# Kernel optimization log

Measured on AMD Instinct MI355X. Metric: run time of the kernel, lower is better.

The kernel has to match this reference:

```python
import jax, jax.numpy as jnp
import numpy as np

IN_DIM = 512
HID = IN_DIM // 2
N_SCENES = 64
SEG_LEN = 4096
N = N_SCENES * SEG_LEN
EPS = 1e-5


def setup_inputs() -> dict:
    key = jax.random.key(0)
    ks = jax.random.split(key, 6)
    feats = jax.random.normal(ks[0], (N, IN_DIM), dtype=jnp.float32)
    offsets = (jnp.arange(N_SCENES + 1, dtype=jnp.int32) * SEG_LEN)
    ln_g = jnp.ones((IN_DIM,), jnp.float32) + 0.02 * jax.random.normal(ks[1], (IN_DIM,), jnp.float32)
    ln_b = 0.02 * jax.random.normal(ks[2], (IN_DIM,), jnp.float32)
    w1 = jax.random.normal(ks[3], (HID, IN_DIM), jnp.float32) / np.sqrt(IN_DIM)
    b1 = jnp.zeros((HID,), jnp.float32)
    w2 = jax.random.normal(ks[4], (1, HID), jnp.float32) / np.sqrt(HID)
    b2 = jnp.zeros((1,), jnp.float32)
    return {"feats": feats, "ln_g": ln_g, "ln_b": ln_b, "w1": w1, "b1": b1, "w2": w2, "b2": b2, "offsets": offsets}


def reference(feats, ln_g, ln_b, w1, b1, w2, b2, offsets):
    n = feats.shape[0]
    # segment id per point from prefix-sum offsets
    seg = jnp.searchsorted(offsets, jnp.arange(n, dtype=offsets.dtype), side="right") - 1
    # score MLP: LayerNorm -> Linear -> GELU(exact) -> Linear -> scalar
    mu = jnp.mean(feats, axis=-1, keepdims=True)
    var = jnp.mean(jnp.square(feats - mu), axis=-1, keepdims=True)
    x = (feats - mu) * jax.lax.rsqrt(var + EPS) * ln_g + ln_b
    h = jax.nn.gelu(x @ w1.T + b1, approximate=False)  # [N, HID]
    s = (h @ w2.T + b2)[:, 0]  # [N]
    # segment softmax (stable)
    smax = jax.ops.segment_max(s, seg, num_segments=N_SCENES)
    e = jnp.exp(s - smax[seg])
    denom = jax.ops.segment_sum(e, seg, num_segments=N_SCENES)
    w = e / denom[seg]
    # weighted sum per segment -> [N_SCENES, IN_DIM]
    pooled = jax.ops.segment_sum(feats * w[:, None], seg, num_segments=N_SCENES)
    return pooled
```

## Files before the change

kernel.cpp:

```cpp
#include <hip/hip_runtime.h>

#define IN_DIM 512
#define HID_DIM 256

typedef __bf16 bf16x8 __attribute__((ext_vector_type(8)));
typedef unsigned short ushort8 __attribute__((ext_vector_type(8)));
typedef float floatx4 __attribute__((ext_vector_type(4)));

__device__ __forceinline__ unsigned short f2bf(float x) {
    unsigned int u = __float_as_uint(x);
    u += 0x7FFFu + ((u >> 16) & 1u);
    return (unsigned short)(u >> 16);
}

__global__ void conv_w1_kernel(const float* __restrict__ w1,
                               unsigned short* __restrict__ w1bf, int n) {
    int i = blockIdx.x * blockDim.x + threadIdx.x;
    if (i < n) w1bf[i] = f2bf(w1[i]);
}

#define XS_STRIDE 520

__global__ __launch_bounds__(256, 2) void score_kernel(
    const float* __restrict__ feats, const float* __restrict__ ln_g,
    const float* __restrict__ ln_b, const unsigned short* __restrict__ w1bf,
    const float* __restrict__ b1, const float* __restrict__ w2,
    const float* __restrict__ b2, float* __restrict__ s_out, int N) {
    __shared__ unsigned short xs[64][XS_STRIDE];
    __shared__ float spart[4][64];

    const int tid = threadIdx.x;
    const int wid = tid >> 6;
    const int lane = tid & 63;
    const int quad = lane >> 4;
    const int l16 = lane & 15;
    const int row0 = blockIdx.x * 64;
    const int c8 = lane * 8;

    const float4 g0 = *(const float4*)(ln_g + c8);
    const float4 g1 = *(const float4*)(ln_g + c8 + 4);
    const float4 h0 = *(const float4*)(ln_b + c8);
    const float4 h1 = *(const float4*)(ln_b + c8 + 4);

    for (int i = 0; i < 16; i += 2) {
        const int ra = (wid << 4) + i;
        const int rb = ra + 1;
        size_t rowa = (size_t)(row0 + ra);
        size_t rowb = (size_t)(row0 + rb);
        if (rowa >= (size_t)N) rowa = (size_t)N - 1;
        if (rowb >= (size_t)N) rowb = (size_t)N - 1;
        const float4 a0 = *(const float4*)(feats + rowa * IN_DIM + c8);
        const float4 a1 = *(const float4*)(feats + rowa * IN_DIM + c8 + 4);
        const float4 d0 = *(const float4*)(feats + rowb * IN_DIM + c8);
        const float4 d1 = *(const float4*)(feats + rowb * IN_DIM + c8 + 4);

        float sa = a0.x + a0.y + a0.z + a0.w + a1.x + a1.y + a1.z + a1.w;
        float qa = a0.x * a0.x + a0.y * a0.y + a0.z * a0.z + a0.w * a0.w +
                   a1.x * a1.x + a1.y * a1.y + a1.z * a1.z + a1.w * a1.w;
        float sb = d0.x + d0.y + d0.z + d0.w + d1.x + d1.y + d1.z + d1.w;
        float qb = d0.x * d0.x + d0.y * d0.y + d0.z * d0.z + d0.w * d0.w +
                   d1.x * d1.x + d1.y * d1.y + d1.z * d1.z + d1.w * d1.w;
        for (int m = 32; m; m >>= 1) {
            sa += __shfl_xor(sa, m);
            qa += __shfl_xor(qa, m);
            sb += __shfl_xor(sb, m);
            qb += __shfl_xor(qb, m);
        }
        const float mua = sa * (1.0f / IN_DIM);
        const float rsa = rsqrtf(qa * (1.0f / IN_DIM) - mua * mua + 1e-5f);
        const float mub = sb * (1.0f / IN_DIM);
        const float rsb = rsqrtf(qb * (1.0f / IN_DIM) - mub * mub + 1e-5f);

        ushort8 va, vb;
        va[0] = f2bf((a0.x - mua) * rsa * g0.x + h0.x);
        va[1] = f2bf((a0.y - mua) * rsa * g0.y + h0.y);
        va[2] = f2bf((a0.z - mua) * rsa * g0.z + h0.z);
        va[3] = f2bf((a0.w - mua) * rsa * g0.w + h0.w);
        va[4] = f2bf((a1.x - mua) * rsa * g1.x + h1.x);
        va[5] = f2bf((a1.y - mua) * rsa * g1.y + h1.y);
        va[6] = f2bf((a1.z - mua) * rsa * g1.z + h1.z);
        va[7] = f2bf((a1.w - mua) * rsa * g1.w + h1.w);
        vb[0] = f2bf((d0.x - mub) * rsb * g0.x + h0.x);
        vb[1] = f2bf((d0.y - mub) * rsb * g0.y + h0.y);
        vb[2] = f2bf((d0.z - mub) * rsb * g0.z + h0.z);
        vb[3] = f2bf((d0.w - mub) * rsb * g0.w + h0.w);
        vb[4] = f2bf((d1.x - mub) * rsb * g1.x + h1.x);
        vb[5] = f2bf((d1.y - mub) * rsb * g1.y + h1.y);
        vb[6] = f2bf((d1.z - mub) * rsb * g1.z + h1.z);
        vb[7] = f2bf((d1.w - mub) * rsb * g1.w + h1.w);
        *(ushort8*)&xs[ra][c8] = va;
        *(ushort8*)&xs[rb][c8] = vb;
    }
    __syncthreads();

    floatx4 acc[4][4];
#pragma unroll
    for (int rt = 0; rt < 4; rt++)
#pragma unroll
        for (int ht = 0; ht < 4; ht++) acc[rt][ht] = (floatx4)(0.0f);

    const int hbase = wid * 64;
    for (int kk = 0; kk < IN_DIM; kk += 32) {
        const int kc = kk + quad * 8;
        bf16x8 af[4], bf[4];
#pragma unroll
        for (int rt = 0; rt < 4; rt++) {
            af[rt] = __builtin_bit_cast(bf16x8, *(const ushort8*)&xs[rt * 16 + l16][kc]);
        }
#pragma unroll
        for (int ht = 0; ht < 4; ht++) {
            const int hid = hbase + ht * 16 + l16;
            bf[ht] = __builtin_bit_cast(bf16x8, *(const ushort8*)(w1bf + hid * IN_DIM + kc));
        }
#pragma unroll
        for (int rt = 0; rt < 4; rt++)
#pragma unroll
            for (int ht = 0; ht < 4; ht++)
                acc[rt][ht] = __builtin_amdgcn_mfma_f32_16x16x32_bf16(af[rt], bf[ht], acc[rt][ht], 0, 0, 0);
    }
    __syncthreads();

    float w2v[4], b1v[4];
#pragma unroll
    for (int ht = 0; ht < 4; ht++) {
        const int hid = hbase + ht * 16 + l16;
        w2v[ht] = w2[hid];
        b1v[ht] = b1[hid];
    }
    float p[4][4];
#pragma unroll
    for (int rt = 0; rt < 4; rt++) {
#pragma unroll
        for (int reg = 0; reg < 4; reg++) {
            float t = 0.0f;
#pragma unroll
            for (int ht = 0; ht < 4; ht++) {
                const float hv = acc[rt][ht][reg] + b1v[ht];
                t += 0.5f * hv * (1.0f + erff(hv * 0.70710678118654752f)) * w2v[ht];
            }
            p[rt][reg] = t;
        }
    }
#pragma unroll
    for (int m = 1; m < 16; m <<= 1)
#pragma unroll
        for (int rt = 0; rt < 4; rt++)
#pragma unroll
            for (int reg = 0; reg < 4; reg++) p[rt][reg] += __shfl_xor(p[rt][reg], m);
    if (l16 == 0) {
#pragma unroll
        for (int rt = 0; rt < 4; rt++)
#pragma unroll
            for (int reg = 0; reg < 4; reg++)
                spart[wid][rt * 16 + quad * 4 + reg] = p[rt][reg];
    }
    __syncthreads();
    if (tid < 64) {
        const int row = row0 + tid;
        if (row < N) {
            s_out[row] = spart[0][tid] + spart[1][tid] + spart[2][tid] + spart[3][tid] + b2[0];
        }
    }
}

__global__ void segstat_kernel(const float* __restrict__ s, const int* __restrict__ offsets,
                               float* __restrict__ smax, float* __restrict__ denom, int nseg) {
    const int seg = blockIdx.x;
    const int st = offsets[seg];
    const int en = offsets[seg + 1];
    const int tid = threadIdx.x;
    __shared__ float red[8];
    float m = -3.4e38f;
    for (int i = st + tid; i < en; i += 256) m = fmaxf(m, s[i]);
    for (int mm = 32; mm; mm >>= 1) m = fmaxf(m, __shfl_xor(m, mm));
    if ((tid & 63) == 0) red[tid >> 6] = m;
    __syncthreads();
    const float M = fmaxf(fmaxf(red[0], red[1]), fmaxf(red[2], red[3]));
    float sum = 0.0f;
    for (int i = st + tid; i < en; i += 256) sum += expf(s[i] - M);
    for (int mm = 32; mm; mm >>= 1) sum += __shfl_xor(sum, mm);
    if ((tid & 63) == 0) red[4 + (tid >> 6)] = sum;
    __syncthreads();
    if (tid == 0) {
        smax[seg] = M;
        denom[seg] = red[4] + red[5] + red[6] + red[7];
    }
}

#define CHUNK 512
__global__ __launch_bounds__(256) void pool_kernel(
    const float* __restrict__ feats, const float* __restrict__ s,
    const float* __restrict__ smax, const float* __restrict__ denom,
    const int* __restrict__ offsets, int nseg, float* __restrict__ out, int N) {
    __shared__ float wbuf[CHUNK];
    __shared__ int sbuf[CHUNK];
    const int tid = threadIdx.x;
    const int r0 = blockIdx.x * CHUNK;
    const int nrows = min(CHUNK, N - r0);

    for (int r = tid; r < CHUNK; r += 256) {
        const int row = r0 + r;
        float wv = 0.0f;
        int sg = 0;
        if (row < N) {
            int lo = 0, hi = nseg;
            while (hi - lo > 1) {
                const int mid = (lo + hi) >> 1;
                if (offsets[mid] <= row) lo = mid; else hi = mid;
            }
            sg = lo;
            wv = expf(s[row] - smax[sg]) / denom[sg];
        }
        wbuf[r] = wv;
        sbuf[r] = sg;
    }
    __syncthreads();

    const int seg0 = sbuf[0];
    const int segl = sbuf[nrows - 1];
    const int d = 2 * tid;
    if (seg0 == segl) {
        float ax = 0.0f, ay = 0.0f;
        const float* fp = feats + (size_t)r0 * IN_DIM + d;
#pragma unroll 8
        for (int r = 0; r < nrows; r++) {
            const float2 f = *(const float2*)(fp + (size_t)r * IN_DIM);
            const float wv = wbuf[r];
            ax += wv * f.x;
            ay += wv * f.y;
        }
        atomicAdd(&out[seg0 * IN_DIM + d], ax);
        atomicAdd(&out[seg0 * IN_DIM + d + 1], ay);
    } else {
        for (int r = 0; r < nrows; r++) {
            const float2 f = *(const float2*)(feats + (size_t)(r0 + r) * IN_DIM + d);
            const float wv = wbuf[r];
            const int sg = sbuf[r];
            if (wv != 0.0f) {
                atomicAdd(&out[sg * IN_DIM + d], wv * f.x);
                atomicAdd(&out[sg * IN_DIM + d + 1], wv * f.y);
            }
        }
    }
}

extern "C" void kernel_launch(void* const* d_in, const int* in_sizes, int n_in,
                              void* d_out, int out_size, void* d_ws, size_t ws_size,
                              hipStream_t stream) {
    const float* feats = (const float*)d_in[0];
    const float* ln_g = (const float*)d_in[1];
    const float* ln_b = (const float*)d_in[2];
    const float* w1 = (const float*)d_in[3];
    const float* b1 = (const float*)d_in[4];
    const float* w2 = (const float*)d_in[5];
    const float* b2 = (const float*)d_in[6];
    const int* offsets = (const int*)d_in[7];
    const int N = in_sizes[0] / IN_DIM;
    const int nseg = in_sizes[7] - 1;
    float* out = (float*)d_out;

    char* ws = (char*)d_ws;
    unsigned short* w1bf = (unsigned short*)ws;
    float* s_arr = (float*)(ws + (size_t)HID_DIM * IN_DIM * 2);
    float* smax = (float*)(ws + (size_t)HID_DIM * IN_DIM * 2 + (size_t)N * 4);
    float* denom = smax + nseg;

    hipMemsetAsync(d_out, 0, (size_t)out_size * sizeof(float), stream);
    conv_w1_kernel<<<(HID_DIM * IN_DIM + 255) / 256, 256, 0, stream>>>(w1, w1bf, HID_DIM * IN_DIM);
    score_kernel<<<(N + 63) / 64, 256, 0, stream>>>(feats, ln_g, ln_b, w1bf, b1, w2, b2, s_arr, N);
    segstat_kernel<<<nseg, 256, 0, stream>>>(s_arr, offsets, smax, denom, nseg);
    pool_kernel<<<(N + CHUNK - 1) / CHUNK, 256, 0, stream>>>(feats, s_arr, smax, denom, offsets, nseg, out, N);
}
```

Measured before the change: 943.3 us.

## Fold LayerNorm affine into W1 and apply normalization after the GEMM

Pre-multiplies W1 by the LayerNorm gain and precomputes per-hidden sums of the scaled weights and a combined bias that absorbs ln_b and b1. The score kernel now converts raw feats to bf16 without normalizing, and computes per-row mean and variance from the bf16 values read during the MFMA loop. It then applies mean subtraction and rsqrt scaling to the GEMM output in the epilogue, which removes the per-row shuffle reductions and per-element normalize math from the load phase. The trade is extra precision loss: bf16 rounding of un-normalized feats, statistics taken from bf16 values, and cancellation in acc minus mu times gw. The pool kernel chunk size is also halved to 256.

New measurement: 941.0 us. Within noise of the previous version (-0.2%).

```diff
diff --git a/kernel.cpp b/kernel.cpp
--- a/kernel.cpp
+++ b/kernel.cpp
@@ -2,32 +2,65 @@
 
 #define IN_DIM 512
 #define HID_DIM 256
+#define XS_STRIDE 520
 
 typedef __bf16 bf16x8 __attribute__((ext_vector_type(8)));
 typedef unsigned short ushort8 __attribute__((ext_vector_type(8)));
 typedef float floatx4 __attribute__((ext_vector_type(4)));
 
-__device__ __forceinline__ unsigned short f2bf(float x) {
+__device__ __forceinline__ unsigned short f2bf_rne(float x) {
     unsigned int u = __float_as_uint(x);
     u += 0x7FFFu + ((u >> 16) & 1u);
     return (unsigned short)(u >> 16);
 }
 
-__global__ void conv_w1_kernel(const float* __restrict__ w1,
-                               unsigned short* __restrict__ w1bf, int n) {
-    int i = blockIdx.x * blockDim.x + threadIdx.x;
-    if (i < n) w1bf[i] = f2bf(w1[i]);
-}
-
-#define XS_STRIDE 520
+__device__ __forceinline__ unsigned int pack_bf2(float lo, float hi) {
+    const unsigned int u0 = __float_as_uint(lo) + 0x8000u;
+    const unsigned int u1 = __float_as_uint(hi) + 0x8000u;
+    return __builtin_amdgcn_perm(u1, u0, 0x07060302u);
+}
+
+__global__ void prep_w1_kernel(const float* __restrict__ w1, const float* __restrict__ ln_g,
+                               const float* __restrict__ ln_b, const float* __restrict__ b1,
+                               unsigned short* __restrict__ w1g, float* __restrict__ gw,
+                               float* __restrict__ c1) {
+    const int wid = threadIdx.x >> 6;
+    const int lane = threadIdx.x & 63;
+    const int h = blockIdx.x * 4 + wid;
+    const int c8 = lane * 8;
+    const float4 wv0 = *(const float4*)(w1 + (size_t)h * IN_DIM + c8);
+    const float4 wv1 = *(const float4*)(w1 + (size_t)h * IN_DIM + c8 + 4);
+    const float4 g0 = *(const float4*)(ln_g + c8);
+    const float4 g1 = *(const float4*)(ln_g + c8 + 4);
+    const float4 bb0 = *(const float4*)(ln_b + c8);
+    const float4 bb1 = *(const float4*)(ln_b + c8 + 4);
+    float wg[8] = {wv0.x * g0.x, wv0.y * g0.y, wv0.z * g0.z, wv0.w * g0.w,
+                   wv1.x * g1.x, wv1.y * g1.y, wv1.z * g1.z, wv1.w * g1.w};
+    float sg = wg[0] + wg[1] + wg[2] + wg[3] + wg[4] + wg[5] + wg[6] + wg[7];
+    float sb = wv0.x * bb0.x + wv0.y * bb0.y + wv0.z * bb0.z + wv0.w * bb0.w +
+               wv1.x * bb1.x + wv1.y * bb1.y + wv1.z * bb1.z + wv1.w * bb1.w;
+    ushort8 outv;
+#pragma unroll
+    for (int j = 0; j < 8; j++) outv[j] = f2bf_rne(wg[j]);
+    *(ushort8*)(w1g + (size_t)h * IN_DIM + c8) = outv;
+    for (int m = 32; m; m >>= 1) {
+        sg += __shfl_xor(sg, m);
+        sb += __shfl_xor(sb, m);
+    }
+    if (lane == 0) {
+        gw[h] = sg;
+        c1[h] = sb + b1[h];
+    }
+}
 
 __global__ __launch_bounds__(256, 2) void score_kernel(
-    const float* __restrict__ feats, const float* __restrict__ ln_g,
-    const float* __restrict__ ln_b, const unsigned short* __restrict__ w1bf,
-    const float* __restrict__ b1, const float* __restrict__ w2,
-    const float* __restrict__ b2, float* __restrict__ s_out, int N) {
+    const float* __restrict__ feats, const unsigned short* __restrict__ w1g,
+    const float* __restrict__ gw, const float* __restrict__ c1,
+    const float* __restrict__ w2, const float* __restrict__ b2,
+    float* __restrict__ s_out, int N) {
     __shared__ unsigned short xs[64][XS_STRIDE];
     __shared__ float spart[4][64];
+    __shared__ float2 stats_s[64];
 
     const int tid = threadIdx.x;
     const int wid = tid >> 6;
@@ -37,59 +70,28 @@
     const int row0 = blockIdx.x * 64;
     const int c8 = lane * 8;
 
-    const float4 g0 = *(const float4*)(ln_g + c8);
-    const float4 g1 = *(const float4*)(ln_g + c8 + 4);
-    const float4 h0 = *(const float4*)(ln_b + c8);
-    const float4 h1 = *(const float4*)(ln_b + c8 + 4);
-
+#pragma unroll 4
     for (int i = 0; i < 16; i += 2) {
         const int ra = (wid << 4) + i;
-        const int rb = ra + 1;
         size_t rowa = (size_t)(row0 + ra);
-        size_t rowb = (size_t)(row0 + rb);
+        size_t rowb = rowa + 1;
         if (rowa >= (size_t)N) rowa = (size_t)N - 1;
         if (rowb >= (size_t)N) rowb = (size_t)N - 1;
         const float4 a0 = *(const float4*)(feats + rowa * IN_DIM + c8);
         const float4 a1 = *(const float4*)(feats + rowa * IN_DIM + c8 + 4);
         const float4 d0 = *(const float4*)(feats + rowb * IN_DIM + c8);
         const float4 d1 = *(const float4*)(feats + rowb * IN_DIM + c8 + 4);
-
-        float sa = a0.x + a0.y + a0.z + a0.w + a1.x + a1.y + a1.z + a1.w;
-        float qa = a0.x * a0.x + a0.y * a0.y + a0.z * a0.z + a0.w * a0.w +
-                   a1.x * a1.x + a1.y * a1.y + a1.z * a1.z + a1.w * a1.w;
-        float sb = d0.x + d0.y + d0.z + d0.w + d1.x + d1.y + d1.z + d1.w;
-        float qb = d0.x * d0.x + d0.y * d0.y + d0.z * d0.z + d0.w * d0.w +
-                   d1.x * d1.x + d1.y * d1.y + d1.z * d1.z + d1.w * d1.w;
-        for (int m = 32; m; m >>= 1) {
-            sa += __shfl_xor(sa, m);
-            qa += __shfl_xor(qa, m);
-            sb += __shfl_xor(sb, m);
-            qb += __shfl_xor(qb, m);
-        }
-        const float mua = sa * (1.0f / IN_DIM);
-        const float rsa = rsqrtf(qa * (1.0f / IN_DIM) - mua * mua + 1e-5f);
-        const float mub = sb * (1.0f / IN_DIM);
-        const float rsb = rsqrtf(qb * (1.0f / IN_DIM) - mub * mub + 1e-5f);
-
-        ushort8 va, vb;
-        va[0] = f2bf((a0.x - mua) * rsa * g0.x + h0.x);
-        va[1] = f2bf((a0.y - mua) * rsa * g0.y + h0.y);
-        va[2] = f2bf((a0.z - mua) * rsa * g0.z + h0.z);
-        va[3] = f2bf((a0.w - mua) * rsa * g0.w + h0.w);
-        va[4] = f2bf((a1.x - mua) * rsa * g1.x + h1.x);
-        va[5] = f2bf((a1.y - mua) * rsa * g1.y + h1.y);
-        va[6] = f2bf((a1.z - mua) * rsa * g1.z + h1.z);
-        va[7] = f2bf((a1.w - mua) * rsa * g1.w + h1.w);
-        vb[0] = f2bf((d0.x - mub) * rsb * g0.x + h0.x);
-        vb[1] = f2bf((d0.y - mub) * rsb * g0.y + h0.y);
-        vb[2] = f2bf((d0.z - mub) * rsb * g0.z + h0.z);
-        vb[3] = f2bf((d0.w - mub) * rsb * g0.w + h0.w);
-        vb[4] = f2bf((d1.x - mub) * rsb * g1.x + h1.x);
-        vb[5] = f2bf((d1.y - mub) * rsb * g1.y + h1.y);
-        vb[6] = f2bf((d1.z - mub) * rsb * g1.z + h1.z);
-        vb[7] = f2bf((d1.w - mub) * rsb * g1.w + h1.w);
-        *(ushort8*)&xs[ra][c8] = va;
-        *(ushort8*)&xs[rb][c8] = vb;
+        uint4 pa, pb;
+        pa.x = pack_bf2(a0.x, a0.y);
+        pa.y = pack_bf2(a0.z, a0.w);
+        pa.z = pack_bf2(a1.x, a1.y);
+        pa.w = pack_bf2(a1.z, a1.w);
+        pb.x = pack_bf2(d0.x, d0.y);
+        pb.y = pack_bf2(d0.z, d0.w);
+        pb.z = pack_bf2(d1.x, d1.y);
+        pb.w = pack_bf2(d1.z, d1.w);
+        *(uint4*)&xs[ra][c8] = pa;
+        *(uint4*)&xs[ra + 1][c8] = pb;
     }
     __syncthreads();
 
@@ -99,43 +101,74 @@
 #pragma unroll
         for (int ht = 0; ht < 4; ht++) acc[rt][ht] = (floatx4)(0.0f);
 
+    float sumf = 0.0f, sumq = 0.0f;
     const int hbase = wid * 64;
     for (int kk = 0; kk < IN_DIM; kk += 32) {
         const int kc = kk + quad * 8;
-        bf16x8 af[4], bf[4];
+        ushort8 au[4];
+        bf16x8 bf[4];
 #pragma unroll
         for (int rt = 0; rt < 4; rt++) {
-            af[rt] = __builtin_bit_cast(bf16x8, *(const ushort8*)&xs[rt * 16 + l16][kc]);
+            au[rt] = *(const ushort8*)&xs[rt * 16 + l16][kc];
+            if (rt == wid) {
+                const unsigned int* p = (const unsigned int*)&au[rt];
+#pragma unroll
+                for (int d = 0; d < 4; d++) {
+                    const float lo = __uint_as_float(p[d] << 16);
+                    const float hi = __uint_as_float(p[d] & 0xffff0000u);
+                    sumf += lo + hi;
+                    sumq += lo * lo + hi * hi;
+                }
+            }
         }
 #pragma unroll
         for (int ht = 0; ht < 4; ht++) {
             const int hid = hbase + ht * 16 + l16;
-            bf[ht] = __builtin_bit_cast(bf16x8, *(const ushort8*)(w1bf + hid * IN_DIM + kc));
+            bf[ht] = __builtin_bit_cast(bf16x8, *(const ushort8*)(w1g + hid * IN_DIM + kc));
         }
 #pragma unroll
         for (int rt = 0; rt < 4; rt++)
 #pragma unroll
             for (int ht = 0; ht < 4; ht++)
-                acc[rt][ht] = __builtin_amdgcn_mfma_f32_16x16x32_bf16(af[rt], bf[ht], acc[rt][ht], 0, 0, 0);
-    }
-    __syncthreads();
-
-    float w2v[4], b1v[4];
+                acc[rt][ht] = __builtin_amdgcn_mfma_f32_16x16x32_bf16(
+                    __builtin_bit_cast(bf16x8, au[rt]), bf[ht], acc[rt][ht], 0, 0, 0);
+    }
+
+    sumf += __shfl_xor(sumf, 16);
+    sumf += __shfl_xor(sumf, 32);
+    sumq += __shfl_xor(sumq, 16);
+    sumq += __shfl_xor(sumq, 32);
+    if (lane < 16) {
+        const float mu = sumf * (1.0f / IN_DIM);
+        const float var = fmaxf(sumq * (1.0f / IN_DIM) - mu * mu, 0.0f);
+        stats_s[(wid << 4) + lane] = make_float2(mu, rsqrtf(var + 1e-5f));
+    }
+    __syncthreads();
+
+    float gwv[4], c1v[4], w2v[4];
 #pragma unroll
     for (int ht = 0; ht < 4; ht++) {
         const int hid = hbase + ht * 16 + l16;
+        gwv[ht] = gw[hid];
+        c1v[ht] = c1[hid];
         w2v[ht] = w2[hid];
-        b1v[ht] = b1[hid];
-    }
+    }
+    float2 st[4][4];
+#pragma unroll
+    for (int rt = 0; rt < 4; rt++)
+#pragma unroll
+        for (int reg = 0; reg < 4; reg++) st[rt][reg] = stats_s[rt * 16 + quad * 4 + reg];
+
     float p[4][4];
 #pragma unroll
     for (int rt = 0; rt < 4; rt++) {
 #pragma unroll
         for (int reg = 0; reg < 4; reg++) {
+            const float mu = st[rt][reg].x, rs = st[rt][reg].y;
             float t = 0.0f;
 #pragma unroll
             for (int ht = 0; ht < 4; ht++) {
-                const float hv = acc[rt][ht][reg] + b1v[ht];
+                const float hv = rs * (acc[rt][ht][reg] - mu * gwv[ht]) + c1v[ht];
                 t += 0.5f * hv * (1.0f + erff(hv * 0.70710678118654752f)) * w2v[ht];
             }
             p[rt][reg] = t;
@@ -157,9 +190,8 @@
     __syncthreads();
     if (tid < 64) {
         const int row = row0 + tid;
-        if (row < N) {
+        if (row < N)
             s_out[row] = spart[0][tid] + spart[1][tid] + spart[2][tid] + spart[3][tid] + b2[0];
-        }
     }
 }
 
@@ -187,7 +219,7 @@
     }
 }
 
-#define CHUNK 512
+#define CHUNK 256
 __global__ __launch_bounds__(256) void pool_kernel(
     const float* __restrict__ feats, const float* __restrict__ s,
     const float* __restrict__ smax, const float* __restrict__ denom,
@@ -198,8 +230,8 @@
     const int r0 = blockIdx.x * CHUNK;
     const int nrows = min(CHUNK, N - r0);
 
-    for (int r = tid; r < CHUNK; r += 256) {
-        const int row = r0 + r;
+    {
+        const int row = r0 + tid;
         float wv = 0.0f;
         int sg = 0;
         if (row < N) {
@@ -211,8 +243,8 @@
             sg = lo;
             wv = expf(s[row] - smax[sg]) / denom[sg];
         }
-        wbuf[r] = wv;
-        sbuf[r] = sg;
+        wbuf[tid] = wv;
+        sbuf[tid] = sg;
     }
     __syncthreads();
 
@@ -260,14 +292,16 @@
     float* out = (float*)d_out;
 
     char* ws = (char*)d_ws;
-    unsigned short* w1bf = (unsigned short*)ws;
-    float* s_arr = (float*)(ws + (size_t)HID_DIM * IN_DIM * 2);
-    float* smax = (float*)(ws + (size_t)HID_DIM * IN_DIM * 2 + (size_t)N * 4);
+    unsigned short* w1g = (unsigned short*)ws;
+    float* gw = (float*)(ws + (size_t)HID_DIM * IN_DIM * 2);
+    float* c1 = gw + HID_DIM;
+    float* s_arr = c1 + HID_DIM;
+    float* smax = s_arr + N;
     float* denom = smax + nseg;
 
     hipMemsetAsync(d_out, 0, (size_t)out_size * sizeof(float), stream);
-    conv_w1_kernel<<<(HID_DIM * IN_DIM + 255) / 256, 256, 0, stream>>>(w1, w1bf, HID_DIM * IN_DIM);
-    score_kernel<<<(N + 63) / 64, 256, 0, stream>>>(feats, ln_g, ln_b, w1bf, b1, w2, b2, s_arr, N);
+    prep_w1_kernel<<<HID_DIM / 4, 256, 0, stream>>>(w1, ln_g, ln_b, b1, w1g, gw, c1);
+    score_kernel<<<(N + 63) / 64, 256, 0, stream>>>(feats, w1g, gw, c1, w2, b2, s_arr, N);
     segstat_kernel<<<nseg, 256, 0, stream>>>(s_arr, offsets, smax, denom, nseg);
     pool_kernel<<<(N + CHUNK - 1) / CHUNK, 256, 0, stream>>>(feats, s_arr, smax, denom, offsets, nseg, out, N);
 }
```
